# Kernel tuning notes

Measured on AMD Instinct MI355X. Metric: run time of the kernel, lower is better.

The kernel has to match this reference:

```python
import jax, jax.numpy as jnp
import numpy as np

IN_F, H1, H2, NC = 784, 1024, 1024, 10
BATCH = 32
EPS = 0.1


def setup_inputs() -> dict:
    key = jax.random.key(0)
    ks = jax.random.split(key, 8)
    x = jax.random.normal(ks[0], (BATCH, IN_F), jnp.float32)
    y = jax.random.randint(ks[1], (BATCH,), 0, NC)
    W1 = jax.random.normal(ks[2], (H1, IN_F), jnp.float32) / np.float32(np.sqrt(IN_F))
    b1 = jax.random.normal(ks[3], (H1,), jnp.float32) * 0.01
    W2 = jax.random.normal(ks[4], (H2, H1), jnp.float32) / np.float32(np.sqrt(H1))
    b2 = jax.random.normal(ks[5], (H2,), jnp.float32) * 0.01
    W3 = jax.random.normal(ks[6], (NC, H2), jnp.float32) / np.float32(np.sqrt(H2))
    b3 = jax.random.normal(ks[7], (NC,), jnp.float32) * 0.01
    return dict(x=x, y=y, W1=W1, b1=b1, W2=W2, b2=b2, W3=W3, b3=b3)


def _relu_coeffs(zl, zu):
    # d = 1 where zl>=0, zu/(zu-zl) where crossing, 0 where zu<=0 (as in select_layer)
    I = (zl < 0) & (zu > 0)
    d = jnp.where(zl >= 0, 1.0, jnp.where(I, zu / (zu - zl), 0.0))
    lI = jnp.where(I, zl, 0.0)  # zl restricted to crossing set I
    return d, lI


def reference(x, y, W1, b1, W2, b2, W3, b3):
    eps = jnp.float32(EPS)
    # ---- layer-1 preactivation bounds (InfBall fval) ----
    nom1 = x @ W1.T + b1                              # [B,H1]
    r1 = eps * jnp.abs(W1).sum(1)                     # [H1]
    zl1, zu1 = nom1 - r1, nom1 + r1
    d1, l1m = _relu_coeffs(zl1, zu1)                  # [B,H1]

    # ---- layer-2 preactivation bounds via dual (transpose) propagation, nu = I ----
    nu1 = W2[None, :, :] * d1[:, None, :]             # [B,H2,H1]  (D1 W2^T rows)
    V0 = jnp.einsum('bji,ik->bjk', nu1, W1)           # [B,H2,IN]
    A = jnp.einsum('bjk,bk->bj', V0, x) + b2 + nu1 @ b1
    E = eps * jnp.abs(V0).sum(-1)
    crossl = jnp.einsum('bji,bi->bj', jax.nn.relu(-nu1), l1m)
    crossu = jnp.einsum('bji,bi->bj', jax.nn.relu(nu1), l1m)
    zl2 = A - E + crossl
    zu2 = A + E - crossu
    d2, l2m = _relu_coeffs(zl2, zu2)                  # [B,H2]

    # ---- final robust bounds: c[b,j,:] = e_{y_b} - e_j ----
    eye = jnp.eye(NC, dtype=x.dtype)
    c = eye[y][:, None, :] - eye[None, :, :]          # [B,NC,NC]
    nu2 = (c @ W3) * d2[:, None, :]                   # [B,NC,H2]
    nu1f = (nu2 @ W2) * d1[:, None, :]                # [B,NC,H1]
    V0f = nu1f @ W1                                   # [B,NC,IN]
    Af = jnp.einsum('bjk,bk->bj', V0f, x) + c @ b3 + nu2 @ b2 + nu1f @ b1
    Ef = eps * jnp.abs(V0f).sum(-1)
    crossf = (jnp.einsum('bji,bi->bj', jax.nn.relu(-nu2), l2m)
              + jnp.einsum('bji,bi->bj', jax.nn.relu(-nu1f), l1m))
    J = Af - Ef + crossf                              # lower bound of c^T z
    return -J                                         # f: upper bound of z_j - z_y, [B,NC]
```

## Files before the change

### kernel.cpp

```cpp
#include <hip/hip_runtime.h>
#include <math.h>

#define B    32
#define INF  784
#define H1   1024
#define H2   1024
#define NC   10
#define EPSV 0.1f

typedef __attribute__((ext_vector_type(8))) short short8;
typedef __attribute__((ext_vector_type(4))) float floatx4;

__device__ inline ushort bf16_rne(float f) {
  uint u = __builtin_bit_cast(uint, f);
  u += 0x7FFFu + ((u >> 16) & 1u);
  return (ushort)(u >> 16);
}
__device__ inline uint pack2(float a, float b) {
  return (uint)bf16_rne(a) | ((uint)bf16_rne(b) << 16);
}
__device__ inline uint scale_pack(uint u, float d0, float d1v) {
  float f0 = __builtin_bit_cast(float, u << 16) * d0;
  float f1 = __builtin_bit_cast(float, u & 0xFFFF0000u) * d1v;
  uint r0 = __builtin_bit_cast(uint, f0) + 0x8000u;
  uint r1 = __builtin_bit_cast(uint, f1) + 0x8000u;
  return __builtin_amdgcn_perm(r1, r0, 0x07060302u);
}

__global__ __launch_bounds__(256) void k_pre(
    const float* __restrict__ x, const float* __restrict__ W1,
    const float* __restrict__ b1, const float* __restrict__ W2,
    ushort* __restrict__ W1F, ushort* __restrict__ W2F,
    float* __restrict__ d1B, float* __restrict__ t1B, float* __restrict__ dnB,
    float* __restrict__ Ezero)
{
  __shared__ float red[4][B + 1];
  __shared__ float Ts[4][32][17];
  int bid = blockIdx.x;
  int t = threadIdx.x;
  if (bid < 64) {
    int jt = bid;
    int lane = t & 63, c0 = t >> 6;
    int l15 = lane & 15, quad = lane >> 4;
    for (int c = c0; c < 32; c += 4) {
      const float* src = &W2[(size_t)(jt * 16 + l15) * H1 + c * 32 + quad * 8];
      float4 v0 = *reinterpret_cast<const float4*>(src);
      float4 v1 = *reinterpret_cast<const float4*>(src + 4);
      uint4 o;
      o.x = pack2(v0.x, v0.y); o.y = pack2(v0.z, v0.w);
      o.z = pack2(v1.x, v1.y); o.w = pack2(v1.z, v1.w);
      *reinterpret_cast<uint4*>(&W2F[((size_t)(c * 64 + jt) * 64 + lane) * 8]) = o;
    }
  } else if (bid < 113) {
    int mt = bid - 64;
    int col0 = mt * 16;
    int w = t >> 6, lane = t & 63;
    int l15 = lane & 15, quad = lane >> 4;
    for (int cg = 0; cg < 8; cg++) {
      int c = cg * 4 + w;
#pragma unroll
      for (int p = 0; p < 8; p++) {
        int r = p * 4 + (lane >> 4);
        Ts[w][r][lane & 15] = W1[(size_t)(c * 32 + r) * INF + col0 + (lane & 15)];
      }
      float f[8];
#pragma unroll
      for (int e = 0; e < 8; e++) f[e] = Ts[w][quad * 8 + e][l15];
      uint4 o;
      o.x = pack2(f[0], f[1]); o.y = pack2(f[2], f[3]);
      o.z = pack2(f[4], f[5]); o.w = pack2(f[6], f[7]);
      *reinterpret_cast<uint4*>(&W1F[((size_t)(c * 49 + mt) * 64 + lane) * 8]) = o;
    }
  } else if (bid < 1137) {
    int i = bid - 113;
    const float* w = W1 + (size_t)i * INF;
    float acc[B];
#pragma unroll
    for (int b = 0; b < B; b++) acc[b] = 0.f;
    float wabs = 0.f;
    for (int k = t; k < INF; k += 256) {
      float wv = w[k];
      wabs += fabsf(wv);
#pragma unroll
      for (int b = 0; b < B; b++) acc[b] = fmaf(x[b * INF + k], wv, acc[b]);
    }
#pragma unroll
    for (int off = 32; off > 0; off >>= 1) {
#pragma unroll
      for (int b = 0; b < B; b++) acc[b] += __shfl_down(acc[b], off, 64);
      wabs += __shfl_down(wabs, off, 64);
    }
    int wave = t >> 6, lane = t & 63;
    if (lane == 0) {
#pragma unroll
      for (int b = 0; b < B; b++) red[wave][b] = acc[b];
      red[wave][B] = wabs;
    }
    __syncthreads();
    if (t < B) {
      float s = red[0][t] + red[1][t] + red[2][t] + red[3][t];
      float r = EPSV * (red[0][B] + red[1][B] + red[2][B] + red[3][B]);
      float nom = s + b1[i];
      float zl = nom - r, zu = nom + r;
      float d, l;
      if (zl >= 0.f)      { d = 1.f;            l = 0.f; }
      else if (zu > 0.f)  { d = zu / (zu - zl); l = zl;  }
      else                { d = 0.f;            l = 0.f; }
      d1B[(size_t)t * H1 + i] = d;
      t1B[(size_t)t * H1 + i] = d * l;
      dnB[(size_t)t * H1 + i] = d * nom;
    }
  } else {
    int zb = bid - 1137;
    for (int idx = t; idx < 8192; idx += 256) {
      int pos = zb * 8192 + idx;
      if (pos < 54272) Ezero[pos] = 0.f;
    }
  }
}

#define K3_LOAD(c, A, Bv) do {                                                  \
  _Pragma("unroll")                                                             \
  for (int ni = 0; ni < 2; ni++)                                                \
    Bv[ni] = *reinterpret_cast<const uint4*>(bBase + (size_t)(c) * 32768 + ni * 512); \
  _Pragma("unroll")                                                             \
  for (int mi = 0; mi < 7; mi++)                                                \
    A[mi] = *reinterpret_cast<const uint4*>(aBase + (size_t)(c) * 25088 + mi * 512); \
} while (0)

#define K3F_COMP(c, A, Bv) do {                                                 \
  float4 dv0 = *reinterpret_cast<const float4*>(&Ds[(c) * 32 + quad * 8]);      \
  float4 dv1 = *reinterpret_cast<const float4*>(&Ds[(c) * 32 + quad * 8 + 4]);  \
  short8 bfr[2];                                                                \
  _Pragma("unroll")                                                             \
  for (int ni = 0; ni < 2; ni++) {                                              \
    uint4 sb;                                                                   \
    sb.x = scale_pack(Bv[ni].x, dv0.x, dv0.y);                                  \
    sb.y = scale_pack(Bv[ni].y, dv0.z, dv0.w);                                  \
    sb.z = scale_pack(Bv[ni].z, dv1.x, dv1.y);                                  \
    sb.w = scale_pack(Bv[ni].w, dv1.z, dv1.w);                                  \
    bfr[ni] = __builtin_bit_cast(short8, sb);                                   \
  }                                                                             \
  _Pragma("unroll")                                                             \
  for (int mi = 0; mi < 7; mi++) {                                              \
    short8 af = __builtin_bit_cast(short8, A[mi]);                              \
    _Pragma("unroll")                                                           \
    for (int ni = 0; ni < 2; ni++)                                              \
      acc[mi][ni] = __builtin_amdgcn_mfma_f32_16x16x32_bf16(af, bfr[ni], acc[mi][ni], 0, 0, 0); \
  }                                                                             \
} while (0)

__global__ __launch_bounds__(256, 3) void k3(
    const ushort* __restrict__ W1F, const ushort* __restrict__ W2F,
    const float* __restrict__ d1B, float* __restrict__ E)
{
  int b = blockIdx.z;
  int t = threadIdx.x, w = t >> 6, lane = t & 63;
  int quad = lane >> 4, l15 = lane & 15;
  int mt0 = blockIdx.x * 7;
  int jt0 = blockIdx.y * 8 + w * 2;

  __shared__ float Ds[H1];
  for (int idx = t; idx < H1; idx += 256) Ds[idx] = d1B[(size_t)b * H1 + idx];
  __syncthreads();

  const ushort* aBase = W1F + ((size_t)mt0 * 64 + lane) * 8;
  const ushort* bBase = W2F + ((size_t)jt0 * 64 + lane) * 8;

  floatx4 acc[7][2];
#pragma unroll
  for (int mi = 0; mi < 7; mi++)
#pragma unroll
    for (int ni = 0; ni < 2; ni++) acc[mi][ni] = (floatx4){0.f, 0.f, 0.f, 0.f};

  uint4 a0[7], b0[2], a1[7], b1v[2];
  K3_LOAD(0, a0, b0);
  K3_LOAD(1, a1, b1v);
  for (int c = 0; c < 30; c += 2) {
    K3F_COMP(c, a0, b0);
    K3_LOAD(c + 2, a0, b0);
    K3F_COMP(c + 1, a1, b1v);
    if (c + 3 < 32) K3_LOAD(c + 3, a1, b1v);
  }
  K3F_COMP(30, a0, b0);
  K3F_COMP(31, a1, b1v);

#pragma unroll
  for (int ni = 0; ni < 2; ni++) {
    float s = 0.f;
#pragma unroll
    for (int mi = 0; mi < 7; mi++)
#pragma unroll
      for (int r = 0; r < 4; r++) s += fabsf(acc[mi][ni][r]);
    s += __shfl_xor(s, 16, 64);
    s += __shfl_xor(s, 32, 64);
    if (lane < 16) {
      int j = (jt0 + ni) * 16 + l15;
      atomicAdd(&E[(size_t)j * B + b], EPSV * s);
    }
  }
}

__global__ __launch_bounds__(256) void k245a(
    const float* __restrict__ W2, const float* __restrict__ b2,
    const float* __restrict__ dnB, const float* __restrict__ t1B,
    const float* __restrict__ E, const float* __restrict__ W3,
    const int* __restrict__ y,
    float* __restrict__ nu2T, float* __restrict__ F2)
{
  int j = blockIdx.x;
  int t = threadIdx.x;
  int wave = t >> 6, lane = t & 63;
  int b0 = wave * 8;
  float aA[8] = {}, aCl[8] = {}, aCu[8] = {};
  const float* __restrict__ w2 = W2 + (size_t)j * H1;
  for (int i = lane; i < H1; i += 64) {
    float wv = w2[i];
    float wp = fmaxf(wv, 0.f), wn = fmaxf(-wv, 0.f);
#pragma unroll
    for (int r = 0; r < 8; r++) {
      float dv = dnB[(size_t)(b0 + r) * H1 + i];
      float tv = t1B[(size_t)(b0 + r) * H1 + i];
      aA[r]  = fmaf(wv, dv, aA[r]);
      aCl[r] = fmaf(wn, tv, aCl[r]);
      aCu[r] = fmaf(wp, tv, aCu[r]);
    }
  }
#pragma unroll
  for (int off = 32; off > 0; off >>= 1) {
#pragma unroll
    for (int r = 0; r < 8; r++) {
      aA[r]  += __shfl_down(aA[r],  off, 64);
      aCl[r] += __shfl_down(aCl[r], off, 64);
      aCu[r] += __shfl_down(aCu[r], off, 64);
    }
  }
  __shared__ float sA[B], sCl[B], sCu[B];
  __shared__ float sd2[B], st2[B], sdb[B], swy[B], sw3[NC];
  float bj = b2[j];
  if (lane == 0) {
#pragma unroll
    for (int r = 0; r < 8; r++) {
      sA [b0 + r] = aA[r] + bj;
      sCl[b0 + r] = aCl[r];
      sCu[b0 + r] = aCu[r];
    }
  }
  if (t >= 64 && t < 96)   swy[t - 64]  = W3[(size_t)y[t - 64] * H2 + j];
  if (t >= 128 && t < 138) sw3[t - 128] = W3[(size_t)(t - 128) * H2 + j];
  __syncthreads();
  if (t < B) {
    float a = sA[t], e = E[(size_t)j * B + t];
    float zl = a - e + sCl[t];
    float zu = a + e - sCu[t];
    float d, l;
    if (zl >= 0.f)      { d = 1.f;            l = 0.f; }
    else if (zu > 0.f)  { d = zu / (zu - zl); l = zl;  }
    else                { d = 0.f;            l = 0.f; }
    sd2[t] = d;
    st2[t] = d * l;
    sdb[t] = d * bj;
  }
  __syncthreads();
  for (int tt = t; tt < B * NC; tt += 256) {
    int b = tt / NC, jc = tt - b * NC;
    float cw = swy[b] - sw3[jc];
    float d2v = sd2[b];
    nu2T[((size_t)b * H2 + j) * 12 + jc] = cw * d2v;
    float val = cw * sdb[b] + fmaxf(-cw, 0.f) * st2[b];
    atomicAdd(&F2[((size_t)(j & 63) * B + b) * NC + jc], val);
  }
}

__global__ __launch_bounds__(256) void k5b1(
    const float* __restrict__ W2, const float* __restrict__ nu2T,
    float* __restrict__ hpart)
{
  int t = threadIdx.x;
  int i1 = blockIdx.x * 512 + t * 2;
  int b = blockIdx.y, s = blockIdx.z;
  const float* __restrict__ nrowb = nu2T + ((size_t)b * H2 + s * 128) * 12;
  const float* __restrict__ w2b = W2 + (size_t)s * 128 * H1 + i1;
  float h0[NC] = {}, h1[NC] = {};
  for (int i2 = 0; i2 < 128; i2++) {
    float2 wv = *reinterpret_cast<const float2*>(&w2b[(size_t)i2 * H1]);
    const float* __restrict__ nrow = nrowb + i2 * 12;
#pragma unroll
    for (int j = 0; j < NC; j++) {
      h0[j] = fmaf(nrow[j], wv.x, h0[j]);
      h1[j] = fmaf(nrow[j], wv.y, h1[j]);
    }
  }
#pragma unroll
  for (int j = 0; j < NC; j++) {
    float2 o; o.x = h0[j]; o.y = h1[j];
    *reinterpret_cast<float2*>(&hpart[(((size_t)s * B + b) * NC + j) * H1 + i1]) = o;
  }
}

__global__ __launch_bounds__(256) void k5b2(
    const float* __restrict__ hpart,
    const float* __restrict__ d1B, const float* __restrict__ t1B,
    const float* __restrict__ dnB,
    float* __restrict__ nu1fT, float* __restrict__ F)
{
  int t = threadIdx.x;
  int i1 = blockIdx.x * 256 + t;
  int b = blockIdx.y;
  float d1v = d1B[(size_t)b * H1 + i1];
  float t1v = t1B[(size_t)b * H1 + i1];
  float dnv = dnB[(size_t)b * H1 + i1];
  float sn[NC], c1[NC];
#pragma unroll
  for (int j = 0; j < NC; j++) {
    float hv = 0.f;
#pragma unroll
    for (int s = 0; s < 8; s++)
      hv += hpart[(((size_t)s * B + b) * NC + j) * H1 + i1];
    nu1fT[((size_t)b * H1 + i1) * 12 + j] = hv * d1v;
    sn[j] = hv * dnv;
    c1[j] = fmaxf(-hv, 0.f) * t1v;
  }
#pragma unroll
  for (int off = 32; off > 0; off >>= 1) {
#pragma unroll
    for (int j = 0; j < NC; j++) {
      sn[j] += __shfl_down(sn[j], off, 64);
      c1[j] += __shfl_down(c1[j], off, 64);
    }
  }
  __shared__ float red[4][2 * NC];
  int wave = t >> 6, lane = t & 63;
  if (lane == 0) {
#pragma unroll
    for (int j = 0; j < NC; j++) { red[wave][j] = sn[j]; red[wave][NC + j] = c1[j]; }
  }
  __syncthreads();
  if (t < NC) {
    float s = 0.f;
    for (int w = 0; w < 4; w++) s += red[w][t] + red[w][NC + t];
    atomicAdd(&F[b * NC + t], s);
  }
}

__global__ __launch_bounds__(128) void k5c1(
    const float* __restrict__ W1, const float* __restrict__ nu1fT,
    float* __restrict__ ppart)
{
  int t = threadIdx.x;
  bool valid = (t < 112);
  int k = blockIdx.x * 112 + (valid ? t : 0);
  int b = blockIdx.y, s = blockIdx.z;
  const float* __restrict__ nrowb = nu1fT + ((size_t)b * H1 + s * 128) * 12;
  const float* __restrict__ w1b = W1 + (size_t)s * 128 * INF + k;
  float acc[NC] = {};
  for (int i1 = 0; i1 < 128; i1++) {
    float w1v = w1b[(size_t)i1 * INF];
    const float* __restrict__ nrow = nrowb + i1 * 12;
#pragma unroll
    for (int j = 0; j < NC; j++) acc[j] = fmaf(nrow[j], w1v, acc[j]);
  }
  if (valid) {
#pragma unroll
    for (int j = 0; j < NC; j++)
      ppart[(((size_t)s * B + b) * NC + j) * INF + k] = acc[j];
  }
}

__global__ __launch_bounds__(256) void k5c2_out(
    const float* __restrict__ ppart, const float* __restrict__ F,
    const float* __restrict__ F2, const float* __restrict__ b3,
    const int* __restrict__ y, float* __restrict__ out)
{
  int b = blockIdx.x;
  int t = threadIdx.x;
  float e[NC] = {};
  for (int k = t; k < INF; k += 256) {
#pragma unroll
    for (int j = 0; j < NC; j++) {
      float v = 0.f;
#pragma unroll
      for (int s = 0; s < 8; s++)
        v += ppart[(((size_t)s * B + b) * NC + j) * INF + k];
      e[j] += fabsf(v);
    }
  }
#pragma unroll
  for (int off = 32; off > 0; off >>= 1) {
#pragma unroll
    for (int j = 0; j < NC; j++) e[j] += __shfl_down(e[j], off, 64);
  }
  __shared__ float red[4][NC];
  int wave = t >> 6, lane = t & 63;
  if (lane == 0) {
#pragma unroll
    for (int j = 0; j < NC; j++) red[wave][j] = e[j];
  }
  __syncthreads();
  if (t < NC) {
    float ef = 0.f;
    for (int w = 0; w < 4; w++) ef += red[w][t];
    float s = F[b * NC + t];
    for (int slot = 0; slot < 64; slot++)
      s += F2[((size_t)slot * B + b) * NC + t];
    int yb = y[b];
    s += b3[yb] - b3[t];
    out[b * NC + t] = EPSV * ef - s;
  }
}

extern "C" void kernel_launch(void* const* d_in, const int* in_sizes, int n_in,
                              void* d_out, int out_size, void* d_ws, size_t ws_size,
                              hipStream_t stream) {
  const float* x  = (const float*)d_in[0];
  const int*   y  = (const int*)  d_in[1];
  const float* W1 = (const float*)d_in[2];
  const float* b1 = (const float*)d_in[3];
  const float* W2 = (const float*)d_in[4];
  const float* b2 = (const float*)d_in[5];
  const float* W3 = (const float*)d_in[6];
  const float* b3 = (const float*)d_in[7];
  float* out = (float*)d_out;
  float* ws  = (float*)d_ws;

  float* d1B  = ws;
  float* t1B  = ws + 32768;
  float* dnB  = ws + 65536;
  float* E    = ws + 196608;
  float* F    = ws + 229376;
  float* F2   = ws + 230400;
  float* nu2T = ws + 328704;
  ushort* W2F = (ushort*)(ws + 721920);
  ushort* W1F = (ushort*)(ws + 1246208);
  float* nu1fT = ws + 328704;
  float* hpart = ws + 721920;
  float* ppart = ws + 721920;

  k_pre<<<1144, 256, 0, stream>>>(x, W1, b1, W2, W1F, W2F, d1B, t1B, dnB, E);
  k3<<<dim3(7, 8, 32), 256, 0, stream>>>(W1F, W2F, d1B, E);
  k245a<<<H2, 256, 0, stream>>>(W2, b2, dnB, t1B, E, W3, y, nu2T, F2);
  k5b1<<<dim3(2, B, 8), 256, 0, stream>>>(W2, nu2T, hpart);
  k5b2<<<dim3(4, B), 256, 0, stream>>>(hpart, d1B, t1B, dnB, nu1fT, F);
  k5c1<<<dim3(7, B, 8), 128, 0, stream>>>(W1, nu1fT, ppart);
  k5c2_out<<<B, 256, 0, stream>>>(ppart, F, F2, b3, y, out);
}
```

Measured before the change: 225.1 us.

## Move layer-2 bounds and final back-propagation GEMMs onto bf16 MFMA

Replaces the scalar FP32 kernels for the layer-2 nominal/cross terms, the nu2·W2 product and the nu1f·W1 product with bf16 MFMA kernels. The inputs are pre-packed into fragment layouts: a transposed W2, bf16 dn and t1, and bf16 nu2 and nu1f. The relu split of W2 is done with bit masks. This removes the hpart/ppart partial-sum buffers and their reduction kernels, and the final |V0f| sum is now reduced by atomics. The trade-offs are bf16 rounding error on bound terms that feed a ReLU crossing decision, and very few blocks in k24_mfma (16), which may leave most compute units idle.

```diff
diff --git a/kernel.cpp b/kernel.cpp
--- a/kernel.cpp
+++ b/kernel.cpp
@@ -26,11 +26,19 @@
   uint r1 = __builtin_bit_cast(uint, f1) + 0x8000u;
   return __builtin_amdgcn_perm(r1, r0, 0x07060302u);
 }
+__device__ inline void relu_split(uint v, uint& p, uint& m) {
+  uint sl = ((v >> 15) & 1u) - 1u;
+  uint sh = ((v >> 31) & 1u) - 1u;
+  uint keep = (sl & 0xFFFFu) | (sh & 0xFFFF0000u);
+  p = v & keep;
+  m = (v & ~keep) & 0x7FFF7FFFu;
+}
 
 __global__ __launch_bounds__(256) void k_pre(
     const float* __restrict__ x, const float* __restrict__ W1,
     const float* __restrict__ b1, const float* __restrict__ W2,
     ushort* __restrict__ W1F, ushort* __restrict__ W2F,
+    ushort* __restrict__ W2TF, ushort* __restrict__ dnF, ushort* __restrict__ t1F,
     float* __restrict__ d1B, float* __restrict__ t1B, float* __restrict__ dnB,
     float* __restrict__ Ezero)
 {
@@ -38,11 +46,11 @@
   __shared__ float Ts[4][32][17];
   int bid = blockIdx.x;
   int t = threadIdx.x;
+  int w = t >> 6, lane = t & 63;
+  int quad = lane >> 4, l15 = lane & 15;
   if (bid < 64) {
     int jt = bid;
-    int lane = t & 63, c0 = t >> 6;
-    int l15 = lane & 15, quad = lane >> 4;
-    for (int c = c0; c < 32; c += 4) {
+    for (int c = w; c < 32; c += 4) {
       const float* src = &W2[(size_t)(jt * 16 + l15) * H1 + c * 32 + quad * 8];
       float4 v0 = *reinterpret_cast<const float4*>(src);
       float4 v1 = *reinterpret_cast<const float4*>(src + 4);
@@ -54,14 +62,12 @@
   } else if (bid < 113) {
     int mt = bid - 64;
     int col0 = mt * 16;
-    int w = t >> 6, lane = t & 63;
-    int l15 = lane & 15, quad = lane >> 4;
     for (int cg = 0; cg < 8; cg++) {
       int c = cg * 4 + w;
 #pragma unroll
       for (int p = 0; p < 8; p++) {
-        int r = p * 4 + (lane >> 4);
-        Ts[w][r][lane & 15] = W1[(size_t)(c * 32 + r) * INF + col0 + (lane & 15)];
+        int r = p * 4 + quad;
+        Ts[w][r][l15] = W1[(size_t)(c * 32 + r) * INF + col0 + l15];
       }
       float f[8];
 #pragma unroll
@@ -71,15 +77,33 @@
       o.z = pack2(f[4], f[5]); o.w = pack2(f[6], f[7]);
       *reinterpret_cast<uint4*>(&W1F[((size_t)(c * 49 + mt) * 64 + lane) * 8]) = o;
     }
-  } else if (bid < 1137) {
-    int i = bid - 113;
-    const float* w = W1 + (size_t)i * INF;
+  } else if (bid < 177) {
+    int it = bid - 113;
+    int col0 = it * 16;
+    for (int cg = 0; cg < 8; cg++) {
+      int c = cg * 4 + w;
+#pragma unroll
+      for (int p = 0; p < 8; p++) {
+        int r = p * 4 + quad;
+        Ts[w][r][l15] = W2[(size_t)(c * 32 + r) * H1 + col0 + l15];
+      }
+      float f[8];
+#pragma unroll
+      for (int e = 0; e < 8; e++) f[e] = Ts[w][quad * 8 + e][l15];
+      uint4 o;
+      o.x = pack2(f[0], f[1]); o.y = pack2(f[2], f[3]);
+      o.z = pack2(f[4], f[5]); o.w = pack2(f[6], f[7]);
+      *reinterpret_cast<uint4*>(&W2TF[((size_t)(c * 64 + it) * 64 + lane) * 8]) = o;
+    }
+  } else if (bid < 1201) {
+    int i = bid - 177;
+    const float* wr = W1 + (size_t)i * INF;
     float acc[B];
 #pragma unroll
     for (int b = 0; b < B; b++) acc[b] = 0.f;
     float wabs = 0.f;
     for (int k = t; k < INF; k += 256) {
-      float wv = w[k];
+      float wv = wr[k];
       wabs += fabsf(wv);
 #pragma unroll
       for (int b = 0; b < B; b++) acc[b] = fmaf(x[b * INF + k], wv, acc[b]);
@@ -90,11 +114,10 @@
       for (int b = 0; b < B; b++) acc[b] += __shfl_down(acc[b], off, 64);
       wabs += __shfl_down(wabs, off, 64);
     }
-    int wave = t >> 6, lane = t & 63;
     if (lane == 0) {
 #pragma unroll
-      for (int b = 0; b < B; b++) red[wave][b] = acc[b];
-      red[wave][B] = wabs;
+      for (int b = 0; b < B; b++) red[w][b] = acc[b];
+      red[w][B] = wabs;
     }
     __syncthreads();
     if (t < B) {
@@ -106,15 +129,20 @@
       if (zl >= 0.f)      { d = 1.f;            l = 0.f; }
       else if (zu > 0.f)  { d = zu / (zu - zl); l = zl;  }
       else                { d = 0.f;            l = 0.f; }
+      float dn = d * nom, t1 = d * l;
       d1B[(size_t)t * H1 + i] = d;
-      t1B[(size_t)t * H1 + i] = d * l;
-      dnB[(size_t)t * H1 + i] = d * nom;
+      t1B[(size_t)t * H1 + i] = t1;
+      dnB[(size_t)t * H1 + i] = dn;
+      int c = i >> 5, bt = t >> 4;
+      size_t fa = ((size_t)(c * 2 + bt) * 64 + ((t & 15) | (((i >> 3) & 3) << 4))) * 8 + (i & 7);
+      dnF[fa] = bf16_rne(dn);
+      t1F[fa] = bf16_rne(t1);
     }
   } else {
-    int zb = bid - 1137;
+    int zb = bid - 1201;
     for (int idx = t; idx < 8192; idx += 256) {
       int pos = zb * 8192 + idx;
-      if (pos < 54272) Ezero[pos] = 0.f;
+      if (pos < 44544) Ezero[pos] = 0.f;
     }
   }
 }
@@ -201,211 +229,194 @@
   }
 }
 
-__global__ __launch_bounds__(256) void k245a(
-    const float* __restrict__ W2, const float* __restrict__ b2,
-    const float* __restrict__ dnB, const float* __restrict__ t1B,
-    const float* __restrict__ E, const float* __restrict__ W3,
+__global__ __launch_bounds__(256) void k24_mfma(
+    const ushort* __restrict__ W2F, const ushort* __restrict__ dnF,
+    const ushort* __restrict__ t1F, const float* __restrict__ E,
+    const float* __restrict__ b2, const float* __restrict__ W3,
     const int* __restrict__ y,
-    float* __restrict__ nu2T, float* __restrict__ F2)
-{
-  int j = blockIdx.x;
-  int t = threadIdx.x;
-  int wave = t >> 6, lane = t & 63;
-  int b0 = wave * 8;
-  float aA[8] = {}, aCl[8] = {}, aCu[8] = {};
-  const float* __restrict__ w2 = W2 + (size_t)j * H1;
-  for (int i = lane; i < H1; i += 64) {
-    float wv = w2[i];
-    float wp = fmaxf(wv, 0.f), wn = fmaxf(-wv, 0.f);
-#pragma unroll
-    for (int r = 0; r < 8; r++) {
-      float dv = dnB[(size_t)(b0 + r) * H1 + i];
-      float tv = t1B[(size_t)(b0 + r) * H1 + i];
-      aA[r]  = fmaf(wv, dv, aA[r]);
-      aCl[r] = fmaf(wn, tv, aCl[r]);
-      aCu[r] = fmaf(wp, tv, aCu[r]);
-    }
-  }
-#pragma unroll
-  for (int off = 32; off > 0; off >>= 1) {
-#pragma unroll
-    for (int r = 0; r < 8; r++) {
-      aA[r]  += __shfl_down(aA[r],  off, 64);
-      aCl[r] += __shfl_down(aCl[r], off, 64);
-      aCu[r] += __shfl_down(aCu[r], off, 64);
-    }
-  }
-  __shared__ float sA[B], sCl[B], sCu[B];
-  __shared__ float sd2[B], st2[B], sdb[B], swy[B], sw3[NC];
-  float bj = b2[j];
-  if (lane == 0) {
-#pragma unroll
-    for (int r = 0; r < 8; r++) {
-      sA [b0 + r] = aA[r] + bj;
-      sCl[b0 + r] = aCl[r];
-      sCu[b0 + r] = aCu[r];
-    }
-  }
-  if (t >= 64 && t < 96)   swy[t - 64]  = W3[(size_t)y[t - 64] * H2 + j];
-  if (t >= 128 && t < 138) sw3[t - 128] = W3[(size_t)(t - 128) * H2 + j];
-  __syncthreads();
-  if (t < B) {
-    float a = sA[t], e = E[(size_t)j * B + t];
-    float zl = a - e + sCl[t];
-    float zu = a + e - sCu[t];
-    float d, l;
-    if (zl >= 0.f)      { d = 1.f;            l = 0.f; }
-    else if (zu > 0.f)  { d = zu / (zu - zl); l = zl;  }
-    else                { d = 0.f;            l = 0.f; }
-    sd2[t] = d;
-    st2[t] = d * l;
-    sdb[t] = d * bj;
-  }
-  __syncthreads();
-  for (int tt = t; tt < B * NC; tt += 256) {
-    int b = tt / NC, jc = tt - b * NC;
-    float cw = swy[b] - sw3[jc];
-    float d2v = sd2[b];
-    nu2T[((size_t)b * H2 + j) * 12 + jc] = cw * d2v;
-    float val = cw * sdb[b] + fmaxf(-cw, 0.f) * st2[b];
-    atomicAdd(&F2[((size_t)(j & 63) * B + b) * NC + jc], val);
-  }
-}
-
-__global__ __launch_bounds__(256) void k5b1(
-    const float* __restrict__ W2, const float* __restrict__ nu2T,
-    float* __restrict__ hpart)
-{
-  int t = threadIdx.x;
-  int i1 = blockIdx.x * 512 + t * 2;
-  int b = blockIdx.y, s = blockIdx.z;
-  const float* __restrict__ nrowb = nu2T + ((size_t)b * H2 + s * 128) * 12;
-  const float* __restrict__ w2b = W2 + (size_t)s * 128 * H1 + i1;
-  float h0[NC] = {}, h1[NC] = {};
-  for (int i2 = 0; i2 < 128; i2++) {
-    float2 wv = *reinterpret_cast<const float2*>(&w2b[(size_t)i2 * H1]);
-    const float* __restrict__ nrow = nrowb + i2 * 12;
-#pragma unroll
-    for (int j = 0; j < NC; j++) {
-      h0[j] = fmaf(nrow[j], wv.x, h0[j]);
-      h1[j] = fmaf(nrow[j], wv.y, h1[j]);
-    }
-  }
-#pragma unroll
-  for (int j = 0; j < NC; j++) {
-    float2 o; o.x = h0[j]; o.y = h1[j];
-    *reinterpret_cast<float2*>(&hpart[(((size_t)s * B + b) * NC + j) * H1 + i1]) = o;
-  }
-}
-
-__global__ __launch_bounds__(256) void k5b2(
-    const float* __restrict__ hpart,
+    ushort* __restrict__ nu2F, float* __restrict__ F2)
+{
+  int t = threadIdx.x, w = t >> 6, lane = t & 63;
+  int quad = lane >> 4, l15 = lane & 15;
+  int mt = blockIdx.x * 4 + w;
+  int j0 = mt * 16;
+
+  floatx4 accP[2], accQ[2], accU[2], accL[2];
+#pragma unroll
+  for (int bt = 0; bt < 2; bt++) {
+    accP[bt] = (floatx4){0.f, 0.f, 0.f, 0.f}; accQ[bt] = accP[bt];
+    accU[bt] = accP[bt]; accL[bt] = accP[bt];
+  }
+  const ushort* aBase = W2F + ((size_t)mt * 64 + lane) * 8;
+
+  for (int c = 0; c < 32; c++) {
+    uint4 av = *reinterpret_cast<const uint4*>(aBase + (size_t)c * 32768);
+    uint4 ap, am;
+    relu_split(av.x, ap.x, am.x);
+    relu_split(av.y, ap.y, am.y);
+    relu_split(av.z, ap.z, am.z);
+    relu_split(av.w, ap.w, am.w);
+    short8 afp = __builtin_bit_cast(short8, ap);
+    short8 afm = __builtin_bit_cast(short8, am);
+#pragma unroll
+    for (int bt = 0; bt < 2; bt++) {
+      uint4 bd = *reinterpret_cast<const uint4*>(dnF + ((size_t)(c * 2 + bt) * 64 + lane) * 8);
+      uint4 bl = *reinterpret_cast<const uint4*>(t1F + ((size_t)(c * 2 + bt) * 64 + lane) * 8);
+      short8 fbd = __builtin_bit_cast(short8, bd);
+      short8 fbl = __builtin_bit_cast(short8, bl);
+      accP[bt] = __builtin_amdgcn_mfma_f32_16x16x32_bf16(afp, fbd, accP[bt], 0, 0, 0);
+      accQ[bt] = __builtin_amdgcn_mfma_f32_16x16x32_bf16(afm, fbd, accQ[bt], 0, 0, 0);
+      accU[bt] = __builtin_amdgcn_mfma_f32_16x16x32_bf16(afp, fbl, accU[bt], 0, 0, 0);
+      accL[bt] = __builtin_amdgcn_mfma_f32_16x16x32_bf16(afm, fbl, accL[bt], 0, 0, 0);
+    }
+  }
+
+  float wyr[4], w3r[NC][4];
+#pragma unroll
+  for (int r = 0; r < 4; r++) {
+    int j = j0 + quad * 4 + r;
+#pragma unroll
+    for (int jc = 0; jc < NC; jc++) w3r[jc][r] = W3[(size_t)jc * H2 + j];
+  }
+  int laneHi = (((mt & 1) * 2 + (quad >> 1)) << 4);
+  int eOff = (quad & 1) * 4;
+#pragma unroll
+  for (int bt = 0; bt < 2; bt++) {
+    int b = bt * 16 + l15;
+    int yb = y[b];
+#pragma unroll
+    for (int r = 0; r < 4; r++) {
+      int j = j0 + quad * 4 + r;
+      wyr[r] = W3[(size_t)yb * H2 + j];
+    }
+    float dd[4], tt2[4], ddb[4];
+#pragma unroll
+    for (int r = 0; r < 4; r++) {
+      int j = j0 + quad * 4 + r;
+      float bj = b2[j];
+      float a = accP[bt][r] - accQ[bt][r] + bj;
+      float e = E[(size_t)j * B + b];
+      float zl = a - e + accL[bt][r];
+      float zu = a + e - accU[bt][r];
+      float d, l;
+      if (zl >= 0.f)      { d = 1.f;            l = 0.f; }
+      else if (zu > 0.f)  { d = zu / (zu - zl); l = zl;  }
+      else                { d = 0.f;            l = 0.f; }
+      dd[r] = d; tt2[r] = d * l; ddb[r] = d * bj;
+    }
+    ushort* nbase = nu2F + ((size_t)b * 32 + (mt >> 1)) * 512;
+#pragma unroll
+    for (int jc = 0; jc < 16; jc++) {
+      ushort4 o;
+      float fv = 0.f;
+      if (jc < NC) {
+        float nu[4];
+#pragma unroll
+        for (int r = 0; r < 4; r++) {
+          float cw = wyr[r] - w3r[jc][r];
+          nu[r] = cw * dd[r];
+          fv += cw * ddb[r] + fmaxf(-cw, 0.f) * tt2[r];
+        }
+        o.x = bf16_rne(nu[0]); o.y = bf16_rne(nu[1]);
+        o.z = bf16_rne(nu[2]); o.w = bf16_rne(nu[3]);
+      } else {
+        o.x = o.y = o.z = o.w = 0;
+      }
+      *reinterpret_cast<ushort4*>(nbase + (size_t)(jc | laneHi) * 8 + eOff) = o;
+      if (jc < NC) {
+        fv += __shfl_xor(fv, 16, 64);
+        fv += __shfl_xor(fv, 32, 64);
+        if (lane < 16) atomicAdd(&F2[((size_t)(mt & 31) * B + b) * NC + jc], fv);
+      }
+    }
+  }
+}
+
+__global__ __launch_bounds__(256) void k5b1_mfma(
+    const ushort* __restrict__ W2TF, const ushort* __restrict__ nu2F,
     const float* __restrict__ d1B, const float* __restrict__ t1B,
     const float* __restrict__ dnB,
-    float* __restrict__ nu1fT, float* __restrict__ F)
-{
-  int t = threadIdx.x;
-  int i1 = blockIdx.x * 256 + t;
+    ushort* __restrict__ nu1fF, float* __restrict__ F)
+{
+  int t = threadIdx.x, w = t >> 6, lane = t & 63;
+  int quad = lane >> 4, l15 = lane & 15;
   int b = blockIdx.y;
-  float d1v = d1B[(size_t)b * H1 + i1];
-  float t1v = t1B[(size_t)b * H1 + i1];
-  float dnv = dnB[(size_t)b * H1 + i1];
-  float sn[NC], c1[NC];
-#pragma unroll
-  for (int j = 0; j < NC; j++) {
-    float hv = 0.f;
-#pragma unroll
-    for (int s = 0; s < 8; s++)
-      hv += hpart[(((size_t)s * B + b) * NC + j) * H1 + i1];
-    nu1fT[((size_t)b * H1 + i1) * 12 + j] = hv * d1v;
-    sn[j] = hv * dnv;
-    c1[j] = fmaxf(-hv, 0.f) * t1v;
-  }
-#pragma unroll
-  for (int off = 32; off > 0; off >>= 1) {
-#pragma unroll
-    for (int j = 0; j < NC; j++) {
-      sn[j] += __shfl_down(sn[j], off, 64);
-      c1[j] += __shfl_down(c1[j], off, 64);
-    }
-  }
-  __shared__ float red[4][2 * NC];
-  int wave = t >> 6, lane = t & 63;
-  if (lane == 0) {
-#pragma unroll
-    for (int j = 0; j < NC; j++) { red[wave][j] = sn[j]; red[wave][NC + j] = c1[j]; }
-  }
-  __syncthreads();
-  if (t < NC) {
-    float s = 0.f;
-    for (int w = 0; w < 4; w++) s += red[w][t] + red[w][NC + t];
-    atomicAdd(&F[b * NC + t], s);
-  }
-}
-
-__global__ __launch_bounds__(128) void k5c1(
-    const float* __restrict__ W1, const float* __restrict__ nu1fT,
-    float* __restrict__ ppart)
-{
-  int t = threadIdx.x;
-  bool valid = (t < 112);
-  int k = blockIdx.x * 112 + (valid ? t : 0);
-  int b = blockIdx.y, s = blockIdx.z;
-  const float* __restrict__ nrowb = nu1fT + ((size_t)b * H1 + s * 128) * 12;
-  const float* __restrict__ w1b = W1 + (size_t)s * 128 * INF + k;
-  float acc[NC] = {};
-  for (int i1 = 0; i1 < 128; i1++) {
-    float w1v = w1b[(size_t)i1 * INF];
-    const float* __restrict__ nrow = nrowb + i1 * 12;
-#pragma unroll
-    for (int j = 0; j < NC; j++) acc[j] = fmaf(nrow[j], w1v, acc[j]);
-  }
-  if (valid) {
-#pragma unroll
-    for (int j = 0; j < NC; j++)
-      ppart[(((size_t)s * B + b) * NC + j) * INF + k] = acc[j];
-  }
-}
-
-__global__ __launch_bounds__(256) void k5c2_out(
-    const float* __restrict__ ppart, const float* __restrict__ F,
-    const float* __restrict__ F2, const float* __restrict__ b3,
+  int mt0 = blockIdx.x * 16 + w * 4;
+
+  floatx4 acc[4];
+#pragma unroll
+  for (int mt = 0; mt < 4; mt++) acc[mt] = (floatx4){0.f, 0.f, 0.f, 0.f};
+
+  for (int c = 0; c < 32; c++) {
+    uint4 bv = *reinterpret_cast<const uint4*>(nu2F + ((size_t)(b * 32 + c)) * 512 + lane * 8);
+    short8 bf = __builtin_bit_cast(short8, bv);
+#pragma unroll
+    for (int mt = 0; mt < 4; mt++) {
+      uint4 av = *reinterpret_cast<const uint4*>(W2TF + ((size_t)(c * 64 + mt0 + mt)) * 512 + lane * 8);
+      acc[mt] = __builtin_amdgcn_mfma_f32_16x16x32_bf16(
+          __builtin_bit_cast(short8, av), bf, acc[mt], 0, 0, 0);
+    }
+  }
+
+  float fs = 0.f;
+#pragma unroll
+  for (int mt = 0; mt < 4; mt++) {
+    int M = mt0 + mt;
+    int i1b = M * 16 + quad * 4;
+    ushort4 o;
+#pragma unroll
+    for (int r = 0; r < 4; r++) {
+      int i1 = i1b + r;
+      float hv = acc[mt][r];
+      float nu = hv * d1B[(size_t)b * H1 + i1];
+      ((ushort*)&o)[r] = bf16_rne(nu);
+      fs += hv * dnB[(size_t)b * H1 + i1] + fmaxf(-hv, 0.f) * t1B[(size_t)b * H1 + i1];
+    }
+    int laneHi = (((M & 1) * 2 + (quad >> 1)) << 4);
+    *reinterpret_cast<ushort4*>(nu1fF + ((size_t)b * 32 + (M >> 1)) * 512 +
+                                (size_t)(l15 | laneHi) * 8 + (quad & 1) * 4) = o;
+  }
+  fs += __shfl_xor(fs, 16, 64);
+  fs += __shfl_xor(fs, 32, 64);
+  if (lane < 16 && l15 < NC) atomicAdd(&F[b * NC + l15], fs);
+}
+
+__global__ __launch_bounds__(256) void k5c1_mfma(
+    const ushort* __restrict__ W1F, const ushort* __restrict__ nu1fF,
+    float* __restrict__ Fef)
+{
+  int t = threadIdx.x, w = t >> 6, lane = t & 63;
+  int l15 = lane & 15;
+  int b = blockIdx.y;
+  int mt = blockIdx.x * 4 + w;
+  if (mt >= 49) return;
+
+  floatx4 acc = (floatx4){0.f, 0.f, 0.f, 0.f};
+  for (int c = 0; c < 32; c++) {
+    uint4 av = *reinterpret_cast<const uint4*>(W1F + ((size_t)(c * 49 + mt) * 64 + lane) * 8);
+    uint4 bv = *reinterpret_cast<const uint4*>(nu1fF + ((size_t)(b * 32 + c)) * 512 + lane * 8);
+    acc = __builtin_amdgcn_mfma_f32_16x16x32_bf16(
+        __builtin_bit_cast(short8, av), __builtin_bit_cast(short8, bv), acc, 0, 0, 0);
+  }
+  float s = fabsf(acc[0]) + fabsf(acc[1]) + fabsf(acc[2]) + fabsf(acc[3]);
+  s += __shfl_xor(s, 16, 64);
+  s += __shfl_xor(s, 32, 64);
+  if (lane < 16 && l15 < NC) atomicAdd(&Fef[b * 16 + l15], s);
+}
+
+__global__ __launch_bounds__(512) void k_out(
+    const float* __restrict__ F, const float* __restrict__ F2,
+    const float* __restrict__ Fef, const float* __restrict__ b3,
     const int* __restrict__ y, float* __restrict__ out)
 {
-  int b = blockIdx.x;
-  int t = threadIdx.x;
-  float e[NC] = {};
-  for (int k = t; k < INF; k += 256) {
-#pragma unroll
-    for (int j = 0; j < NC; j++) {
-      float v = 0.f;
-#pragma unroll
-      for (int s = 0; s < 8; s++)
-        v += ppart[(((size_t)s * B + b) * NC + j) * INF + k];
-      e[j] += fabsf(v);
-    }
-  }
-#pragma unroll
-  for (int off = 32; off > 0; off >>= 1) {
-#pragma unroll
-    for (int j = 0; j < NC; j++) e[j] += __shfl_down(e[j], off, 64);
-  }
-  __shared__ float red[4][NC];
-  int wave = t >> 6, lane = t & 63;
-  if (lane == 0) {
-#pragma unroll
-    for (int j = 0; j < NC; j++) red[wave][j] = e[j];
-  }
-  __syncthreads();
-  if (t < NC) {
-    float ef = 0.f;
-    for (int w = 0; w < 4; w++) ef += red[w][t];
-    float s = F[b * NC + t];
-    for (int slot = 0; slot < 64; slot++)
-      s += F2[((size_t)slot * B + b) * NC + t];
-    int yb = y[b];
-    s += b3[yb] - b3[t];
-    out[b * NC + t] = EPSV * ef - s;
+  int idx = threadIdx.x;
+  if (idx < B * NC) {
+    int b = idx / NC, jc = idx - b * NC;
+    float s = F[b * NC + jc];
+    for (int slot = 0; slot < 32; slot++)
+      s += F2[((size_t)slot * B + b) * NC + jc];
+    s += b3[y[b]] - b3[jc];
+    out[idx] = EPSV * Fef[b * 16 + jc] - s;
   }
 }
 
@@ -423,24 +434,26 @@
   float* out = (float*)d_out;
   float* ws  = (float*)d_ws;
 
-  float* d1B  = ws;
-  float* t1B  = ws + 32768;
-  float* dnB  = ws + 65536;
-  float* E    = ws + 196608;
-  float* F    = ws + 229376;
-  float* F2   = ws + 230400;
-  float* nu2T = ws + 328704;
-  ushort* W2F = (ushort*)(ws + 721920);
-  ushort* W1F = (ushort*)(ws + 1246208);
-  float* nu1fT = ws + 328704;
-  float* hpart = ws + 721920;
-  float* ppart = ws + 721920;
-
-  k_pre<<<1144, 256, 0, stream>>>(x, W1, b1, W2, W1F, W2F, d1B, t1B, dnB, E);
+  float* d1B   = ws;
+  float* t1B   = ws + 32768;
+  float* dnB   = ws + 65536;
+  float* E     = ws + 98304;
+  float* F     = ws + 131072;
+  float* F2    = ws + 132096;
+  float* Fef   = ws + 142336;
+  ushort* W2F   = (ushort*)(ws + 150000);
+  ushort* W1F   = (ushort*)(ws + 674288);
+  ushort* W2TF  = (ushort*)(ws + 1075696);
+  ushort* dnF   = (ushort*)(ws + 1599984);
+  ushort* t1F   = (ushort*)(ws + 1616368);
+  ushort* nu2F  = (ushort*)(ws + 1632752);
+  ushort* nu1fF = (ushort*)(ws + 1894896);
+
+  k_pre<<<1207, 256, 0, stream>>>(x, W1, b1, W2, W1F, W2F, W2TF, dnF, t1F,
+                                  d1B, t1B, dnB, E);
   k3<<<dim3(7, 8, 32), 256, 0, stream>>>(W1F, W2F, d1B, E);
-  k245a<<<H2, 256, 0, stream>>>(W2, b2, dnB, t1B, E, W3, y, nu2T, F2);
-  k5b1<<<dim3(2, B, 8), 256, 0, stream>>>(W2, nu2T, hpart);
-  k5b2<<<dim3(4, B), 256, 0, stream>>>(hpart, d1B, t1B, dnB, nu1fT, F);
-  k5c1<<<dim3(7, B, 8), 128, 0, stream>>>(W1, nu1fT, ppart);
-  k5c2_out<<<B, 256, 0, stream>>>(ppart, F, F2, b3, y, out);
-}
+  k24_mfma<<<16, 256, 0, stream>>>(W2F, dnF, t1F, E, b2, W3, y, nu2F, F2);
+  k5b1_mfma<<<dim3(4, B), 256, 0, stream>>>(W2TF, nu2F, d1B, t1B, dnB, nu1fF, F);
+  k5c1_mfma<<<dim3(13, B), 256, 0, stream>>>(W1F, nu1fF, Fef);
+  k_out<<<1, 512, 0, stream>>>(F, F2, Fef, b3, y, out);
+}
```

Measured after the change: 235.8 us. 4.8% more time.
